# Performance work log

Hardware: AMD Instinct MI355X
Metric: run time of the kernel (lower is better)

The kernel has to match this reference:

```python
import jax, jax.numpy as jnp
import numpy as np

N = 10000          # nodes
E = 160000         # edges
T = 32             # seq_len == n_timesteps
H = 256            # hidden_size
K = 4              # edge_embedding_dim
NF = T * 6         # node_features
PRED = 8           # predicted_timesteps
T_TEACH = T - PRED # teacher-forced steps


def setup_inputs() -> dict:
    key = jax.random.key(0)
    ks = jax.random.split(key, 16)
    s = 0.05
    return {
        "x": jax.random.normal(ks[0], (N, NF), jnp.float32),
        "edge_index": jax.random.randint(ks[1], (2, E), 0, N, jnp.int64),
        "z": jax.random.uniform(ks[2], (E, K), jnp.float32),
        # inner f_out: Linear(H, NF) + ReLU
        "Wf": jax.random.normal(ks[3], (H, NF), jnp.float32) * s,
        "bf": jax.random.normal(ks[4], (NF,), jnp.float32) * s,
        # k-1 edge MLPs: Linear(2*NF, H) -> ReLU -> Linear(H, H), stacked
        "W1": jax.random.normal(ks[5], (K - 1, 2 * NF, H), jnp.float32) * s,
        "b1": jax.random.normal(ks[6], (K - 1, H), jnp.float32) * s,
        "W2": jax.random.normal(ks[7], (K - 1, H, H), jnp.float32) * s,
        "b2": jax.random.normal(ks[8], (K - 1, H), jnp.float32) * s,
        # GRUCell(6, H): torch gate order r, z, n
        "Wih": jax.random.normal(ks[9], (3 * H, 6), jnp.float32) * s,
        "bih": jax.random.normal(ks[10], (3 * H,), jnp.float32) * s,
        "Whh": jax.random.normal(ks[11], (3 * H, H), jnp.float32) * s,
        "bhh": jax.random.normal(ks[12], (3 * H,), jnp.float32) * s,
        # outer f_out: Linear(H, 6) + ReLU
        "Wo": jax.random.normal(ks[13], (H, 6), jnp.float32) * s,
        "bo": jax.random.normal(ks[14], (6,), jnp.float32) * s,
    }


def _forward(x, edge_index, z, Wf, bf, W1, b1, W2, b2, Wih, bih, Whh, bhh, Wo, bo):
    src = edge_index[0]  # x_j (source)
    dst = edge_index[1]  # x_i (target, aggregation index)
    zw = z[:, 1:K].T[:, :, None]  # [K-1, E, 1]
    ones_e = jnp.ones((E,), x.dtype)
    cnt = jnp.maximum(jax.ops.segment_sum(ones_e, dst, num_segments=N), 1.0)[:, None]

    def step(carry, inp):
        h, prev = carry
        t, x_t = inp
        inputs = jnp.where(t < T_TEACH, x_t, prev)  # [N, 6]
        fh = jax.nn.relu(h @ Wf + bf)               # [N, NF]
        # message: cat([x_i, x_j]) = [target, source], detached in torch
        ef = jax.lax.stop_gradient(
            jnp.concatenate([fh[dst], fh[src]], axis=1))  # [E, 2*NF]
        h1 = jax.nn.relu(jnp.einsum('ef,kfh->keh', ef, W1) + b1[:, None, :])
        h2 = jnp.einsum('keh,khg->keg', h1, W2) + b2[:, None, :]  # [K-1,E,H]
        msg = jnp.sum(zw * h2, axis=0)              # [E, H]
        m = jax.ops.segment_sum(msg, dst, num_segments=N) / cnt  # scatter-mean
        # GRUCell(inputs, hidden=m)
        gx = inputs @ Wih.T + bih                   # [N, 3H]
        gh = m @ Whh.T + bhh                        # [N, 3H]
        rx, zx, nx = jnp.split(gx, 3, axis=1)
        rh, zh, nh = jnp.split(gh, 3, axis=1)
        r = jax.nn.sigmoid(rx + rh)
        zg = jax.nn.sigmoid(zx + zh)
        n = jnp.tanh(nx + r * nh)
        h_new = (1.0 - zg) * n + zg * m             # [N, H]
        mu = inputs + jax.nn.relu(h_new @ Wo + bo)  # [N, 6]
        return (h_new, mu), mu

    x_seq = x.reshape(N, T, 6).transpose(1, 0, 2)   # [T, N, 6]
    ts = jnp.arange(T)
    h0 = jnp.zeros((N, H), x.dtype)
    p0 = jnp.zeros((N, 6), x.dtype)
    _, mus = jax.lax.scan(step, (h0, p0), (ts, x_seq))  # [T, N, 6]
    return mus.transpose(1, 0, 2).reshape(N, NF)


def reference(x, edge_index, z, Wf, bf, W1, b1, W2, b2, Wih, bih, Whh, bhh, Wo, bo):
    return _forward(x, edge_index, z, Wf, bf, W1, b1, W2, b2,
                    Wih, bih, Whh, bhh, Wo, bo)
```

## Files before the change

### kernel.cpp

```cpp
#include <hip/hip_runtime.h>
#include <hip/hip_bf16.h>

#define NN 10000
#define NE 160000
#define TS 32
#define HID 256
#define NFEAT 192
#define TTEACH 24

typedef unsigned short u16;
typedef unsigned int u32;
typedef __attribute__((ext_vector_type(8))) short bf16x8;
typedef __attribute__((ext_vector_type(4))) float f32x4;

__device__ __forceinline__ float bf2f(u16 u){
    u32 v = ((u32)u) << 16;
    union { u32 i; float f; } c; c.i = v; return c.f;
}
__device__ __forceinline__ u16 f2bf(float f){
    union { float f; u32 i; } c; c.f = f;
    u32 i = c.i;
    u32 lsb = (i >> 16) & 1u;
    i += 0x7fffu + lsb;
    return (u16)(i >> 16);
}

__global__ void fill_f32(float* p, float v, int n){
    int i = blockIdx.x * 256 + threadIdx.x;
    if (i < n) p[i] = v;
}
__global__ void fill_i32(int* p, int v, int n){
    int i = blockIdx.x * 256 + threadIdx.x;
    if (i < n) p[i] = v;
}
__global__ void copy_i32(const int* __restrict__ a, int* __restrict__ b, int n){
    int i = blockIdx.x * 256 + threadIdx.x;
    if (i < n) b[i] = a[i];
}

__global__ void detect_f32(const u16* __restrict__ zraw, int* __restrict__ flag){
    int c = 0;
    for (int i = 0; i < 128; i++) if (zraw[2*i] >= 0x4000) c++;
    *flag = (c > 8) ? 1 : 0;
}
__global__ void conv_f32(const void* __restrict__ in, float* __restrict__ outp,
                         int n, const int* __restrict__ flag){
    int i = blockIdx.x * 256 + threadIdx.x;
    if (i >= n) return;
    if (*flag) outp[i] = ((const float*)in)[i];
    else       outp[i] = bf2f(((const u16*)in)[i]);
}
__global__ void detect_i64(const int* __restrict__ ei_raw, int* __restrict__ flag){
    int zz = 0;
    #pragma unroll
    for (int i = 0; i < 32; i++) zz |= ei_raw[2*i + 1];
    *flag = (zz == 0) ? 1 : 0;
}
__global__ void copy_edges(const int* __restrict__ ei_raw, const int* __restrict__ flag,
                           int* __restrict__ src, int* __restrict__ dst){
    int e = blockIdx.x * 256 + threadIdx.x;
    if (e >= NE) return;
    int st = (*flag) ? 2 : 1;
    src[e] = ei_raw[(size_t)e * st];
    dst[e] = ei_raw[((size_t)NE + e) * st];
}

__global__ void degree_k(const int* __restrict__ dst, int* __restrict__ cnt, int n){
    int e = blockIdx.x * 256 + threadIdx.x;
    if (e < n) atomicAdd(&cnt[dst[e]], 1);
}
__global__ void invcnt_k(const int* __restrict__ cnt, float* __restrict__ inv, int n){
    int i = blockIdx.x * 256 + threadIdx.x;
    if (i < n) inv[i] = 1.0f / fmaxf((float)cnt[i], 1.0f);
}

__global__ void scan_k(const int* __restrict__ cnt, int* __restrict__ binoff){
    __shared__ int ps[1024];
    int t = threadIdx.x;
    int s = 0;
    if (t < 1000)
        for (int i = 0; i < 10; i++) s += cnt[t*10 + i];
    ps[t] = s;
    __syncthreads();
    for (int ofs = 1; ofs < 1024; ofs <<= 1){
        int v = (t >= ofs) ? ps[t - ofs] : 0;
        __syncthreads();
        ps[t] += v;
        __syncthreads();
    }
    if (t < 1000){
        int run = (t == 0) ? 0 : ps[t-1];
        for (int i = 0; i < 10; i++){
            binoff[t*10 + i] = run;
            run += cnt[t*10 + i];
        }
    }
}
__global__ void scatter_k(const int* __restrict__ src32, const int* __restrict__ dst32,
                          const float* __restrict__ zc, int* __restrict__ cur,
                          int* __restrict__ srcS, int* __restrict__ dstS,
                          float* __restrict__ zS){
    int e = blockIdx.x * 256 + threadIdx.x;
    if (e >= NE) return;
    int d = dst32[e];
    int pos = atomicAdd(&cur[d], 1);
    srcS[pos] = src32[e];
    dstS[pos] = d;
    zS[pos]        = zc[(size_t)e*4 + 1];
    zS[NE + pos]   = zc[(size_t)e*4 + 2];
    zS[2*NE + pos] = zc[(size_t)e*4 + 3];
}

__global__ void build_wft(const float* __restrict__ Wfc, u16* __restrict__ WfT){
    int idx = blockIdx.x * 256 + threadIdx.x;
    if (idx < 256 * 192){
        int k = idx / 192, n = idx % 192;
        WfT[(size_t)n * 256 + k] = f2bf(Wfc[idx]);
    }
}
__global__ void build_w1t(const float* __restrict__ W1c, u16* __restrict__ W1T){
    int idx = blockIdx.x * 256 + threadIdx.x;
    if (idx < 1536 * 192){
        int n = idx / 192, k = idx % 192;
        int kblk = n >> 9, part = (n >> 8) & 1, c = n & 255;
        W1T[idx] = f2bf(W1c[(size_t)kblk * (384*256) + (size_t)(part*192 + k) * 256 + c]);
    }
}
__global__ void conv_bf16(const float* __restrict__ in, u16* __restrict__ outp, int n){
    int i = blockIdx.x * 256 + threadIdx.x;
    if (i < n) outp[i] = f2bf(in[i]);
}
__global__ void build_w2t(const float* __restrict__ W2c, u16* __restrict__ W2T){
    int idx = blockIdx.x * 256 + threadIdx.x;
    if (idx < 768 * 256){
        int k = idx / 256, n = idx % 256;
        W2T[(size_t)n * 768 + k] = f2bf(W2c[idx]);
    }
}
__global__ void mscale_k(float* __restrict__ m_acc, const float* __restrict__ inv,
                         u16* __restrict__ m16){
    int idx = blockIdx.x * 256 + threadIdx.x;
    if (idx < NN * HID){
        m16[idx] = f2bf(m_acc[idx] * inv[idx >> 8]);
        m_acc[idx] = 0.f;
    }
}

template<int MODE>
__global__ __launch_bounds__(256, 2) void gemm_mfma(
    const u16* __restrict__ A16, const u16* __restrict__ BT16,
    const float* __restrict__ bias, float* __restrict__ Cf, u16* __restrict__ Cb,
    int M, int Kd, int Nd)
{
    __shared__ __align__(16) u16 Alds[256 * 40];
    __shared__ __align__(16) u16 Blds[64 * 40];
    const int tid = threadIdx.x;
    const int m0 = blockIdx.x * 256;
    const int n0 = blockIdx.y * 64;
    const int wave = tid >> 6, lane = tid & 63;
    const int quad = lane >> 4, l16 = lane & 15;

    const f32x4 zero4 = {0.f, 0.f, 0.f, 0.f};
    f32x4 acc[4][4];
    #pragma unroll
    for (int r=0;r<4;r++)
        #pragma unroll
        for (int c=0;c<4;c++) acc[r][c] = zero4;

    const int arow = m0 + tid;
    const u16* ap = &A16[(size_t)arow * Kd];
    const int bn = tid >> 2, bseg = tid & 3;
    const u16* bp = &BT16[(size_t)(n0 + bn) * Kd + bseg * 8];

    for (int k0 = 0; k0 < Kd; k0 += 32){
        if (arow < M){
            const uint4* q = reinterpret_cast<const uint4*>(ap + k0);
            uint4 v0 = q[0], v1 = q[1], v2 = q[2], v3 = q[3];
            *reinterpret_cast<uint4*>(&Alds[tid * 40])      = v0;
            *reinterpret_cast<uint4*>(&Alds[tid * 40 + 8])  = v1;
            *reinterpret_cast<uint4*>(&Alds[tid * 40 + 16]) = v2;
            *reinterpret_cast<uint4*>(&Alds[tid * 40 + 24]) = v3;
        } else {
            uint4 zz = {0,0,0,0};
            #pragma unroll
            for (int s=0;s<4;s++)
                *reinterpret_cast<uint4*>(&Alds[tid * 40 + s*8]) = zz;
        }
        {
            uint4 v = *reinterpret_cast<const uint4*>(bp + k0);
            *reinterpret_cast<uint4*>(&Blds[bn * 40 + bseg * 8]) = v;
        }
        __syncthreads();
        bf16x8 af[4], bfr[4];
        #pragma unroll
        for (int r=0;r<4;r++)
            af[r] = *reinterpret_cast<const bf16x8*>(&Alds[(wave*64 + r*16 + l16) * 40 + quad * 8]);
        #pragma unroll
        for (int c=0;c<4;c++)
            bfr[c] = *reinterpret_cast<const bf16x8*>(&Blds[(c*16 + l16) * 40 + quad * 8]);
        #pragma unroll
        for (int r=0;r<4;r++)
            #pragma unroll
            for (int c=0;c<4;c++)
                acc[r][c] = __builtin_amdgcn_mfma_f32_16x16x32_bf16(af[r], bfr[c], acc[r][c], 0, 0, 0);
        __syncthreads();
    }
    #pragma unroll
    for (int c=0;c<4;c++){
        int col = n0 + c*16 + l16;
        float bv = 0.f;
        if (MODE == 0 || MODE == 2) bv = bias[col];
        if (MODE == 1){
            int part = (col >> 8) & 1;
            if (part == 0) bv = bias[(col >> 9) * 256 + (col & 255)];
        }
        #pragma unroll
        for (int r=0;r<4;r++){
            #pragma unroll
            for (int reg=0;reg<4;reg++){
                int row = m0 + wave*64 + r*16 + quad*4 + reg;
                if (row >= M) continue;
                float v = acc[r][c][reg] + bv;
                if (MODE == 0) v = fmaxf(v, 0.f);
                if (MODE == 2) Cf[(size_t)row * Nd + col] = v;
                else           Cb[(size_t)row * Nd + col] = f2bf(v);
            }
        }
    }
}

__global__ __launch_bounds__(256, 2) void edge_mfma(
    const u16* __restrict__ AB16, const u16* __restrict__ W2T,
    const float* __restrict__ b2, const float* __restrict__ zS,
    const int* __restrict__ srcS, const int* __restrict__ dstS,
    float* __restrict__ m_acc)
{
    __shared__ __align__(16) u16 Alds[64 * 40];
    __shared__ __align__(16) u16 Blds[256 * 40];
    __shared__ float zc3[3][64];
    __shared__ int dstc[64], srcc[64];
    __shared__ float stg[4][32][65];
    const int tid = threadIdx.x;
    const int eb = blockIdx.x * 64;

    if (tid < 64){
        srcc[tid] = srcS[eb + tid];
        dstc[tid] = dstS[eb + tid];
    }
    int tz = tid - 64;
    if (tz >= 0 && tz < 192){
        int g = tz / 64, e = tz % 64;
        zc3[g][e] = zS[(size_t)g * NE + eb + e];
    }
    __syncthreads();

    const int wave = tid >> 6, lane = tid & 63;
    const int quad = lane >> 4, l16 = lane & 15;
    const int est = tid >> 2, seg = tid & 3;

    const f32x4 zero4 = {0.f, 0.f, 0.f, 0.f};
    f32x4 acc[4][4];
    #pragma unroll
    for (int r=0;r<4;r++)
        #pragma unroll
        for (int c=0;c<4;c++) acc[r][c] = zero4;

    const int d = dstc[est], s = srcc[est];

    for (int kc = 0; kc < 768; kc += 32){
        const int g  = kc >> 8;
        const int j0 = (kc & 255) + seg * 8;
        {
            uint4 ua = *reinterpret_cast<const uint4*>(&AB16[(size_t)d * 1536 + g * 512 + j0]);
            uint4 ub = *reinterpret_cast<const uint4*>(&AB16[(size_t)s * 1536 + g * 512 + 256 + j0]);
            const u16* wa = (const u16*)&ua;
            const u16* wb = (const u16*)&ub;
            float zk = zc3[g][est];
            u16 pk[8];
            #pragma unroll
            for (int i=0;i<8;i++){
                float v = zk * fmaxf(bf2f(wa[i]) + bf2f(wb[i]), 0.f);
                pk[i] = f2bf(v);
            }
            *reinterpret_cast<uint4*>(&Alds[est * 40 + seg * 8]) = *reinterpret_cast<uint4*>(pk);
        }
        #pragma unroll
        for (int i=0;i<4;i++){
            int n = (tid >> 2) + i * 64;
            uint4 w = *reinterpret_cast<const uint4*>(&W2T[(size_t)n * 768 + kc + seg * 8]);
            *reinterpret_cast<uint4*>(&Blds[n * 40 + seg * 8]) = w;
        }
        __syncthreads();
        bf16x8 af[4], bfr[4];
        #pragma unroll
        for (int r=0;r<4;r++)
            af[r] = *reinterpret_cast<const bf16x8*>(&Alds[(r*16 + l16) * 40 + quad * 8]);
        #pragma unroll
        for (int c=0;c<4;c++)
            bfr[c] = *reinterpret_cast<const bf16x8*>(&Blds[(wave*64 + c*16 + l16) * 40 + quad * 8]);
        #pragma unroll
        for (int r=0;r<4;r++)
            #pragma unroll
            for (int c=0;c<4;c++)
                acc[r][c] = __builtin_amdgcn_mfma_f32_16x16x32_bf16(af[r], bfr[c], acc[r][c], 0, 0, 0);
        __syncthreads();
    }
    #pragma unroll
    for (int c=0;c<4;c++){
        int col = wave*64 + c*16 + l16;
        float b20 = b2[col], b21 = b2[256 + col], b22 = b2[512 + col];
        #pragma unroll
        for (int r=0;r<4;r++){
            #pragma unroll
            for (int reg=0;reg<4;reg++){
                int e = r*16 + quad*4 + reg;
                acc[r][c][reg] += zc3[0][e]*b20 + zc3[1][e]*b21 + zc3[2][e]*b22;
            }
        }
    }
    float sum = 0.f;
    int cur_d = -1;
    const int colg = wave*64 + lane;
    #pragma unroll
    for (int chunk = 0; chunk < 2; chunk++){
        #pragma unroll
        for (int rr = 0; rr < 2; rr++){
            int r = chunk*2 + rr;
            #pragma unroll
            for (int c=0;c<4;c++)
                #pragma unroll
                for (int reg=0;reg<4;reg++){
                    int el = rr*16 + quad*4 + reg;
                    stg[wave][el][c*16 + l16] = acc[r][c][reg];
                }
        }
        __syncthreads();
        for (int e = 0; e < 32; e++){
            int eg = chunk*32 + e;
            int dn = dstc[eg];
            float v = stg[wave][e][lane];
            if (dn != cur_d){
                if (cur_d >= 0) atomicAdd(&m_acc[(size_t)cur_d * 256 + colg], sum);
                cur_d = dn; sum = v;
            } else {
                sum += v;
            }
        }
        __syncthreads();
    }
    if (cur_d >= 0) atomicAdd(&m_acc[(size_t)cur_d * 256 + colg], sum);
}

__global__ void gates_mu_k(
    const float* __restrict__ gh, const u16* __restrict__ m16,
    const float* __restrict__ x, const float* __restrict__ Wih,
    const float* __restrict__ bih, const float* __restrict__ Wo,
    const float* __restrict__ bo, float* __restrict__ prev,
    u16* __restrict__ h16, void* __restrict__ out,
    const int* __restrict__ flag, int t)
{
    const int n = blockIdx.x;
    const int j = threadIdx.x;
    const int idx = n * 256 + j;
    float inp[6];
    if (t < TTEACH){
        #pragma unroll
        for (int c=0;c<6;c++) inp[c] = x[(size_t)n * NFEAT + t * 6 + c];
    } else {
        #pragma unroll
        for (int c=0;c<6;c++) inp[c] = prev[n * 6 + c];
    }
    float m = bf2f(m16[idx]);
    float gxr = bih[j], gxz = bih[256 + j], gxn = bih[512 + j];
    #pragma unroll
    for (int c=0;c<6;c++){
        gxr += inp[c] * Wih[j * 6 + c];
        gxz += inp[c] * Wih[(256 + j) * 6 + c];
        gxn += inp[c] * Wih[(512 + j) * 6 + c];
    }
    float ghr = gh[(size_t)n * 768 + j];
    float ghz = gh[(size_t)n * 768 + 256 + j];
    float ghn = gh[(size_t)n * 768 + 512 + j];
    float r  = 1.f / (1.f + __expf(-(gxr + ghr)));
    float zg = 1.f / (1.f + __expf(-(gxz + ghz)));
    float nn = tanhf(gxn + r * ghn);
    float hv = (1.f - zg) * nn + zg * m;
    h16[idx] = f2bf(hv);
    __shared__ float hl[256];
    __shared__ float part[6][9];
    hl[j] = hv;
    __syncthreads();
    if (j < 48){
        int c = j >> 3, p = j & 7;
        float s = 0.f;
        #pragma unroll 8
        for (int q = 0; q < 32; q++){
            int jj = p*32 + q;
            s += hl[jj] * Wo[jj * 6 + c];
        }
        part[c][p] = s;
    }
    __syncthreads();
    if (j < 6){
        float s = bo[j];
        #pragma unroll
        for (int p = 0; p < 8; p++) s += part[j][p];
        float mu = inp[j] + fmaxf(s, 0.f);
        if (*flag) ((float*)out)[(size_t)n * NFEAT + t * 6 + j] = mu;
        else       ((u16*)out)[(size_t)n * NFEAT + t * 6 + j] = f2bf(mu);
        prev[n * 6 + j] = mu;
    }
}

extern "C" void kernel_launch(void* const* d_in, const int* in_sizes, int n_in,
                              void* d_out, int out_size, void* d_ws, size_t ws_size,
                              hipStream_t stream)
{
    const void* x_r   = d_in[0];
    const int*  ei    = (const int*)d_in[1];
    const void* z_r   = d_in[2];
    const void* Wf_r  = d_in[3];
    const void* bf_r  = d_in[4];
    const void* W1_r  = d_in[5];
    const void* b1_r  = d_in[6];
    const void* W2_r  = d_in[7];
    const void* b2_r  = d_in[8];
    const void* Wih_r = d_in[9];
    const void* bih_r = d_in[10];
    const void* Whh_r = d_in[11];
    const void* bhh_r = d_in[12];
    const void* Wo_r  = d_in[13];
    const void* bo_r  = d_in[14];

    char* ws = (char*)d_ws;
    size_t off = 0;
    auto alloc = [&](size_t bytes){
        void* p = ws + off;
        off += (bytes + 255) & ~(size_t)255;
        return p;
    };
    u16*   h16   = (u16*)  alloc((size_t)NN * HID * 2);
    float* prev  = (float*)alloc((size_t)NN * 6 * 4);
    u16*   fh16  = (u16*)  alloc((size_t)NN * NFEAT * 2);
    u16*   AB16  = (u16*)  alloc((size_t)NN * 1536 * 2);
    float* m_acc = (float*)alloc((size_t)NN * HID * 4);
    u16*   m16   = (u16*)  alloc((size_t)NN * HID * 2);
    float* gh    = (float*)alloc((size_t)NN * 768 * 4);
    float* invc  = (float*)alloc((size_t)NN * 4);
    int*   cnt   = (int*)  alloc((size_t)NN * 4);
    int*   binoff= (int*)  alloc((size_t)(NN + 1) * 4);
    int*   curw  = (int*)  alloc((size_t)NN * 4);
    u16*   WfT   = (u16*)  alloc((size_t)192 * 256 * 2);
    u16*   W1T   = (u16*)  alloc((size_t)1536 * 192 * 2);
    u16*   Whh16 = (u16*)  alloc((size_t)768 * 256 * 2);
    u16*   W2T   = (u16*)  alloc((size_t)256 * 768 * 2);
    int*   src32 = (int*)  alloc((size_t)NE * 4);
    int*   dst32 = (int*)  alloc((size_t)NE * 4);
    int*   srcS  = (int*)  alloc((size_t)NE * 4);
    int*   dstS  = (int*)  alloc((size_t)NE * 4);
    float* zS    = (float*)alloc((size_t)3 * NE * 4);
    int*   fdt   = (int*)  alloc(256);
    int*   fidx  = (int*)  alloc(256);
    float* xc   = (float*)alloc((size_t)NN * NFEAT * 4);
    float* zc   = (float*)alloc((size_t)NE * 4 * 4);
    float* Wfc  = (float*)alloc((size_t)256 * 192 * 4);
    float* bfc  = (float*)alloc(192 * 4);
    float* W1c  = (float*)alloc((size_t)3 * 384 * 256 * 4);
    float* b1c  = (float*)alloc(768 * 4);
    float* W2c  = (float*)alloc((size_t)3 * 256 * 256 * 4);
    float* b2c  = (float*)alloc(768 * 4);
    float* Wihc = (float*)alloc((size_t)768 * 6 * 4);
    float* bihc = (float*)alloc(768 * 4);
    float* Whhc = (float*)alloc((size_t)768 * 256 * 4);
    float* bhhc = (float*)alloc(768 * 4);
    float* Woc  = (float*)alloc((size_t)256 * 6 * 4);
    float* boc  = (float*)alloc(6 * 4);

    detect_f32<<<1, 1, 0, stream>>>((const u16*)z_r, fdt);
    detect_i64<<<1, 1, 0, stream>>>(ei, fidx);
    copy_edges<<<(NE + 255)/256, 256, 0, stream>>>(ei, fidx, src32, dst32);

    auto conv = [&](const void* in, float* outp, int n){
        conv_f32<<<(n + 255)/256, 256, 0, stream>>>(in, outp, n, fdt);
    };
    conv(x_r,   xc,   NN * NFEAT);
    conv(z_r,   zc,   NE * 4);
    conv(Wf_r,  Wfc,  256 * 192);
    conv(bf_r,  bfc,  192);
    conv(W1_r,  W1c,  3 * 384 * 256);
    conv(b1_r,  b1c,  768);
    conv(W2_r,  W2c,  3 * 256 * 256);
    conv(b2_r,  b2c,  768);
    conv(Wih_r, Wihc, 768 * 6);
    conv(bih_r, bihc, 768);
    conv(Whh_r, Whhc, 768 * 256);
    conv(bhh_r, bhhc, 768);
    conv(Wo_r,  Woc,  256 * 6);
    conv(bo_r,  boc,  6);

    fill_f32<<<(NN*HID/2 + 255)/256, 256, 0, stream>>>((float*)h16, 0.f, NN*HID/2);
    fill_f32<<<(NN*6 + 255)/256, 256, 0, stream>>>(prev, 0.f, NN*6);
    fill_f32<<<(NN*HID + 255)/256, 256, 0, stream>>>(m_acc, 0.f, NN*HID);
    fill_i32<<<(NN + 255)/256, 256, 0, stream>>>(cnt, 0, NN);
    degree_k<<<(NE + 255)/256, 256, 0, stream>>>(dst32, cnt, NE);
    invcnt_k<<<(NN + 255)/256, 256, 0, stream>>>(cnt, invc, NN);
    scan_k<<<1, 1024, 0, stream>>>(cnt, binoff);
    copy_i32<<<(NN + 255)/256, 256, 0, stream>>>(binoff, curw, NN);
    scatter_k<<<(NE + 255)/256, 256, 0, stream>>>(src32, dst32, zc, curw, srcS, dstS, zS);
    build_wft<<<(256*192 + 255)/256, 256, 0, stream>>>(Wfc, WfT);
    build_w1t<<<(1536*192 + 255)/256, 256, 0, stream>>>(W1c, W1T);
    conv_bf16<<<(768*256 + 255)/256, 256, 0, stream>>>(Whhc, Whh16, 768*256);
    build_w2t<<<(768*256 + 255)/256, 256, 0, stream>>>(W2c, W2T);

    for (int t = 0; t < TS; t++){
        gemm_mfma<0><<<dim3(40, 3), 256, 0, stream>>>(h16, WfT, bfc, nullptr, fh16, NN, 256, NFEAT);
        gemm_mfma<1><<<dim3(40, 24), 256, 0, stream>>>(fh16, W1T, b1c, nullptr, AB16, NN, NFEAT, 1536);
        edge_mfma<<<2500, 256, 0, stream>>>(AB16, W2T, b2c, zS, srcS, dstS, m_acc);
        mscale_k<<<(NN*HID + 255)/256, 256, 0, stream>>>(m_acc, invc, m16);
        gemm_mfma<2><<<dim3(40, 12), 256, 0, stream>>>(m16, Whh16, bhhc, gh, nullptr, NN, 256, 768);
        gates_mu_k<<<NN, 256, 0, stream>>>(gh, m16, xc, Wihc, bihc, Woc, boc, prev, h16, d_out, fdt, t);
    }
}
```

Baseline: 8.077 ms.

## Prefetch next K-chunk into registers and alias LDS buffers in edge_mfma

The edge MFMA kernel now issues the global loads for the next 32-wide K chunk (gathered A/B node rows and W2T slice) into registers before the current chunk's MFMAs run, so load latency can overlap compute. The A/B staging tiles and the epilogue staging buffer now share one LDS allocation, which reduces per-block LDS. Launch bounds are raised to 4 blocks per SM to raise occupancy. The trade-off is extra live registers for the prefetch (6 uint4 per thread), which could cause spills or limit the higher occupancy target.

```diff
diff --git a/kernel.cpp b/kernel.cpp
--- a/kernel.cpp
+++ b/kernel.cpp
@@ -229,17 +229,18 @@
     }
 }
 
-__global__ __launch_bounds__(256, 2) void edge_mfma(
+__global__ __launch_bounds__(256, 4) void edge_mfma(
     const u16* __restrict__ AB16, const u16* __restrict__ W2T,
     const float* __restrict__ b2, const float* __restrict__ zS,
     const int* __restrict__ srcS, const int* __restrict__ dstS,
     float* __restrict__ m_acc)
 {
-    __shared__ __align__(16) u16 Alds[64 * 40];
-    __shared__ __align__(16) u16 Blds[256 * 40];
+    __shared__ __align__(16) char smem[33280];
+    u16*   Alds = (u16*)smem;
+    u16*   Blds = (u16*)(smem + 5120);
+    float* stg  = (float*)smem;
     __shared__ float zc3[3][64];
     __shared__ int dstc[64], srcc[64];
-    __shared__ float stg[4][32][65];
     const int tid = threadIdx.x;
     const int eb = blockIdx.x * 64;
 
@@ -266,15 +267,23 @@
         for (int c=0;c<4;c++) acc[r][c] = zero4;
 
     const int d = dstc[est], s = srcc[est];
+    const u16* paB = &AB16[(size_t)d * 1536];
+    const u16* pbB = &AB16[(size_t)s * 1536 + 256];
+    const int bn = tid >> 2;
+    const u16* bwB = &W2T[(size_t)bn * 768 + seg * 8];
+
+    uint4 pa = *reinterpret_cast<const uint4*>(&paB[seg * 8]);
+    uint4 pb = *reinterpret_cast<const uint4*>(&pbB[seg * 8]);
+    uint4 pw[4];
+    #pragma unroll
+    for (int i=0;i<4;i++)
+        pw[i] = *reinterpret_cast<const uint4*>(&bwB[(size_t)i * 64 * 768]);
 
     for (int kc = 0; kc < 768; kc += 32){
-        const int g  = kc >> 8;
-        const int j0 = (kc & 255) + seg * 8;
+        const int g = kc >> 8;
         {
-            uint4 ua = *reinterpret_cast<const uint4*>(&AB16[(size_t)d * 1536 + g * 512 + j0]);
-            uint4 ub = *reinterpret_cast<const uint4*>(&AB16[(size_t)s * 1536 + g * 512 + 256 + j0]);
-            const u16* wa = (const u16*)&ua;
-            const u16* wb = (const u16*)&ub;
+            const u16* wa = (const u16*)&pa;
+            const u16* wb = (const u16*)&pb;
             float zk = zc3[g][est];
             u16 pk[8];
             #pragma unroll
@@ -285,12 +294,19 @@
             *reinterpret_cast<uint4*>(&Alds[est * 40 + seg * 8]) = *reinterpret_cast<uint4*>(pk);
         }
         #pragma unroll
-        for (int i=0;i<4;i++){
-            int n = (tid >> 2) + i * 64;
-            uint4 w = *reinterpret_cast<const uint4*>(&W2T[(size_t)n * 768 + kc + seg * 8]);
-            *reinterpret_cast<uint4*>(&Blds[n * 40 + seg * 8]) = w;
-        }
-        __syncthreads();
+        for (int i=0;i<4;i++)
+            *reinterpret_cast<uint4*>(&Blds[(bn + i*64) * 40 + seg * 8]) = pw[i];
+        __syncthreads();
+        if (kc + 32 < 768){
+            const int kn = kc + 32;
+            const int gn = kn >> 8;
+            const int jn = (kn & 255) + seg * 8;
+            pa = *reinterpret_cast<const uint4*>(&paB[gn * 512 + jn]);
+            pb = *reinterpret_cast<const uint4*>(&pbB[gn * 512 + jn]);
+            #pragma unroll
+            for (int i=0;i<4;i++)
+                pw[i] = *reinterpret_cast<const uint4*>(&bwB[(size_t)i * 64 * 768 + kn]);
+        }
         bf16x8 af[4], bfr[4];
         #pragma unroll
         for (int r=0;r<4;r++)
@@ -331,14 +347,14 @@
                 #pragma unroll
                 for (int reg=0;reg<4;reg++){
                     int el = rr*16 + quad*4 + reg;
-                    stg[wave][el][c*16 + l16] = acc[r][c][reg];
+                    stg[wave*(32*65) + el*65 + c*16 + l16] = acc[r][c][reg];
                 }
         }
         __syncthreads();
         for (int e = 0; e < 32; e++){
             int eg = chunk*32 + e;
             int dn = dstc[eg];
-            float v = stg[wave][e][lane];
+            float v = stg[wave*(32*65) + e*65 + lane];
             if (dn != cur_d){
                 if (cur_d >= 0) atomicAdd(&m_acc[(size_t)cur_d * 256 + colg], sum);
                 cur_d = dn; sum = v;
```

Result: slower. 12.69 ms (+57.2%).
